# Kernel tuning notes

Measured on AMD Instinct MI355X. Metric: run time of the kernel, lower is better.

## Reference

```python
import jax, jax.numpy as jnp
import numpy as np

EPS = 0.3
LAYER_NUM = 2
N_NODES = 50000
N_EDGES = 1600000
IN_CH = 256
HIDDEN = 128
OUT_CH = 64


def setup_inputs() -> dict:
    key = jax.random.key(0)
    ks = jax.random.split(key, 8)
    x = jax.random.normal(ks[0], (N_NODES, IN_CH), dtype=jnp.float32)
    edge_index = jax.random.randint(ks[1], (2, N_EDGES), 0, N_NODES, dtype=jnp.int64)
    # xavier-normal-ish scales
    t1_w = jax.random.normal(ks[2], (HIDDEN, IN_CH), dtype=jnp.float32) * (1.414 * (2.0 / (IN_CH + HIDDEN)) ** 0.5)
    t1_b = jnp.zeros((HIDDEN,), dtype=jnp.float32)
    gate_w = jax.random.normal(ks[3], (LAYER_NUM, 2 * HIDDEN), dtype=jnp.float32) * ((2.0 / (2 * HIDDEN + 1)) ** 0.5)
    gate_b = jnp.zeros((LAYER_NUM,), dtype=jnp.float32)
    t2_w = jax.random.normal(ks[4], (OUT_CH, HIDDEN), dtype=jnp.float32) * (1.414 * (2.0 / (HIDDEN + OUT_CH)) ** 0.5)
    t2_b = jnp.zeros((OUT_CH,), dtype=jnp.float32)
    return {"x": x, "edge_index": edge_index, "t1_w": t1_w, "t1_b": t1_b,
            "gate_w": gate_w, "gate_b": gate_b, "t2_w": t2_w, "t2_b": t2_b}


def reference(x, edge_index, t1_w, t1_b, gate_w, gate_b, t2_w, t2_b):
    n = x.shape[0]
    row, col = edge_index[0], edge_index[1]
    # symmetric degree normalization: deg computed over target nodes (row)
    deg = jax.ops.segment_sum(jnp.ones_like(row, dtype=x.dtype), row, num_segments=n)
    dinv = jnp.where(deg > 0, jax.lax.rsqrt(jnp.maximum(deg, 1.0)), 0.0)  # [N]
    edge_norm = dinv[row] * dinv[col]  # [E]

    h = jax.nn.relu(x @ t1_w.T + t1_b)  # [N, H]
    raw = h
    H = h.shape[1]
    for l in range(LAYER_NUM):
        gw_i = gate_w[l, :H]   # weights for h_src (row)
        gw_j = gate_w[l, H:]   # weights for h_dst (col)
        # edge attention g = tanh(gate([h_row || h_col]))  -> [E]
        g = jnp.tanh(h[row] @ gw_i + h[col] @ gw_j + gate_b[l])
        w = g * edge_norm  # [E]
        # scatter-add weighted neighbor features to target nodes
        agg = jax.ops.segment_sum(w[:, None] * h[col], row, num_segments=n)  # [N, H]
        h = EPS * raw + agg
    out = h @ t2_w.T + t2_b  # [N, out]
    return jax.nn.log_softmax(out, axis=1)
```

## Files before the change

### kernel.cpp

```cpp
#include <hip/hip_runtime.h>
#include <math.h>

#define EPSF 0.3f
#define NPB 128
#define SHB 7
#define MAXNB 512
#define CHUNK 4096
#define MAXSEG 8192

typedef __attribute__((ext_vector_type(8))) short bf16x8;
typedef __attribute__((ext_vector_type(4))) float f32x4;

__device__ __forceinline__ uint32_t f2bf(float f) {
    uint32_t u = __float_as_uint(f);
    return (u + 0x7fffu + ((u >> 16) & 1u)) >> 16;
}
__device__ __forceinline__ uint32_t pack2(float lo, float hi) {
    return f2bf(lo) | (f2bf(hi) << 16);
}
__device__ __forceinline__ float bflo(uint32_t u) { return __uint_as_float(u << 16); }
__device__ __forceinline__ float bfhi(uint32_t u) { return __uint_as_float(u & 0xffff0000u); }

__device__ __forceinline__ float fast_tanh(float x) {
    float e = __expf(2.f * x);
    return 1.f - 2.f * __builtin_amdgcn_rcpf(e + 1.f);
}

__device__ __forceinline__ int edge_at(const int* ei, int is64, size_t idx) {
    if (is64) return (int)((const long long*)ei)[idx];
    return ei[idx];
}

__device__ __forceinline__ int detect_is64(const int* ei, int base, int E) {
    __shared__ int s_nz;
    if (threadIdx.x == 0) s_nz = 0;
    __syncthreads();
    int lim = min(512, E - base);
    int nz = 0;
    for (int t = threadIdx.x; t < lim; t += 256)
        nz |= (ei[2 * (size_t)(base + t) + 1] != 0);
    if (nz) atomicOr(&s_nz, 1);
    __syncthreads();
    return s_nz == 0;
}

__global__ __launch_bounds__(256) void k_pack(const int* __restrict__ ei, int E,
                                              uint32_t* __restrict__ pk,
                                              int* __restrict__ hist, int nblk, int NB) {
    __shared__ int lh[MAXNB];
    int base = blockIdx.x * CHUNK;
    int is64 = detect_is64(ei, base, E);
    for (int b = threadIdx.x; b < NB; b += 256) lh[b] = 0;
    __syncthreads();
    for (int j = threadIdx.x; j < CHUNK; j += 256) {
        int e = base + j;
        if (e < E) {
            int r = edge_at(ei, is64, e);
            int c = edge_at(ei, is64, (size_t)E + e);
            pk[e] = ((uint32_t)r << 16) | (uint32_t)c;
            atomicAdd(&lh[r >> SHB], 1);
        }
    }
    __syncthreads();
    for (int b = threadIdx.x; b < NB; b += 256)
        hist[(size_t)b * nblk + blockIdx.x] = lh[b];
}

__global__ void k_scanA(int* __restrict__ hist, int nblk, int* __restrict__ btot) {
    int b = blockIdx.x;
    int lane = threadIdx.x;
    int run = 0;
    for (int seg = 0; seg < nblk; seg += 64) {
        int idx = seg + lane;
        int v = (idx < nblk) ? hist[(size_t)b * nblk + idx] : 0;
        int s = v;
        for (int o = 1; o < 64; o <<= 1) {
            int t = __shfl_up(s, o);
            if (lane >= o) s += t;
        }
        if (idx < nblk) hist[(size_t)b * nblk + idx] = run + s - v;
        run += __shfl(s, 63);
    }
    if (lane == 0) btot[b] = run;
}

__global__ void k_scanB(const int* __restrict__ btot, int NB, int* __restrict__ bbase) {
    __shared__ int s[MAXNB];
    int t = threadIdx.x;
    int v = (t < NB) ? btot[t] : 0;
    s[t] = v;
    __syncthreads();
    for (int o = 1; o < MAXNB; o <<= 1) {
        int x = (t >= o) ? s[t - o] : 0;
        __syncthreads();
        s[t] += x;
        __syncthreads();
    }
    if (t < NB) bbase[t] = s[t] - v;
    if (t == MAXNB - 1) bbase[NB] = s[t];
}

__global__ __launch_bounds__(256) void k_binwrite(const uint32_t* __restrict__ pk, int E,
                                                  const int* __restrict__ hist,
                                                  const int* __restrict__ bbase,
                                                  uint32_t* __restrict__ ebuf,
                                                  int nblk, int NB) {
    __shared__ int lcnt[MAXNB];
    int base = blockIdx.x * CHUNK;
    for (int b = threadIdx.x; b < NB; b += 256)
        lcnt[b] = bbase[b] + hist[(size_t)b * nblk + blockIdx.x];
    __syncthreads();
    for (int j = threadIdx.x; j < CHUNK; j += 256) {
        int e = base + j;
        if (e < E) {
            uint32_t v = __builtin_nontemporal_load(&pk[e]);
            int pos = atomicAdd(&lcnt[v >> (16 + SHB)], 1);
            ebuf[pos] = v;
        }
    }
}

__global__ __launch_bounds__(256) void k_csr(const uint32_t* __restrict__ ebuf,
                                             const int* __restrict__ bbase,
                                             int* __restrict__ rp, float* __restrict__ dinv,
                                             int* __restrict__ ecol, int N, int E, int NB) {
    __shared__ uint32_t seg[MAXSEG];
    __shared__ int cnt[NPB];
    __shared__ int sc[NPB];
    __shared__ int cur[NPB];
    int b = blockIdx.x;
    int tid = threadIdx.x;
    int p0 = bbase[b], p1 = bbase[b + 1];
    int len = p1 - p0;
    bool fits = (len <= MAXSEG);
    int n0 = b << SHB;
    if (tid < NPB) cnt[tid] = 0;
    __syncthreads();
    if (fits) {
        for (int j = tid; j < len; j += 256) {
            uint32_t v = ebuf[p0 + j];
            seg[j] = v;
            atomicAdd(&cnt[(v >> 16) & (NPB - 1)], 1);
        }
    } else {
        for (int j = tid; j < len; j += 256)
            atomicAdd(&cnt[(ebuf[p0 + j] >> 16) & (NPB - 1)], 1);
    }
    __syncthreads();
    if (tid < NPB) sc[tid] = cnt[tid];
    __syncthreads();
    for (int o = 1; o < NPB; o <<= 1) {
        int v = (tid < NPB && tid >= o) ? sc[tid - o] : 0;
        __syncthreads();
        if (tid < NPB) sc[tid] += v;
        __syncthreads();
    }
    if (tid < NPB) {
        int off = sc[tid] - cnt[tid];
        cur[tid] = off;
        int node = n0 + tid;
        if (node < N) {
            rp[node] = p0 + off;
            int d = cnt[tid];
            dinv[node] = d > 0 ? rsqrtf((float)d) : 0.f;
        }
    }
    if (b == NB - 1 && tid == 0) rp[N] = E;
    __syncthreads();
    if (fits) {
        for (int j = tid; j < len; j += 256) {
            uint32_t v = seg[j];
            int pos = p0 + atomicAdd(&cur[(v >> 16) & (NPB - 1)], 1);
            ecol[pos] = (int)(v & 0xffffu);
        }
    } else {
        for (int j = tid; j < len; j += 256) {
            uint32_t v = ebuf[p0 + j];
            int pos = p0 + atomicAdd(&cur[(v >> 16) & (NPB - 1)], 1);
            ecol[pos] = (int)(v & 0xffffu);
        }
    }
}

__global__ __launch_bounds__(256) void k_gemm1(const float* __restrict__ A,
                                               const float* __restrict__ W,
                                               const float* __restrict__ bias,
                                               uint32_t* __restrict__ hb, int M) {
    __shared__ char As[128 * 128];
    __shared__ char Bs[128 * 128];
    const int tid = threadIdx.x;
    const int lane = tid & 63;
    const int wave = tid >> 6;
    const int wr = wave >> 1, wc = wave & 1;
    const int m0 = blockIdx.x * 128;
    const int lrow = lane & 15, lkg = lane >> 4;
    const int sr = tid >> 3;
    const int sc = (tid & 7) * 8;

    f32x4 acc[4][4];
#pragma unroll
    for (int mi = 0; mi < 4; ++mi)
#pragma unroll
        for (int ni = 0; ni < 4; ++ni) acc[mi][ni] = (f32x4){0.f, 0.f, 0.f, 0.f};

    for (int t = 0; t < 4; ++t) {
        const int k0 = t * 64;
#pragma unroll
        for (int i = 0; i < 4; ++i) {
            int r = i * 32 + sr;
            float4 v0 = make_float4(0.f, 0.f, 0.f, 0.f), v1 = v0;
            if (m0 + r < M) {
                const float* p = &A[(size_t)(m0 + r) * 256 + k0 + sc];
                v0 = *(const float4*)p;
                v1 = *(const float4*)(p + 4);
            }
            uint4 pk = make_uint4(pack2(v0.x, v0.y), pack2(v0.z, v0.w),
                                  pack2(v1.x, v1.y), pack2(v1.z, v1.w));
            uint32_t off = (uint32_t)(r * 128 + sc * 2);
            *(uint4*)(As + (off ^ ((r & 7) << 4))) = pk;
        }
#pragma unroll
        for (int i = 0; i < 4; ++i) {
            int r = i * 32 + sr;
            const float* p = &W[(size_t)r * 256 + k0 + sc];
            float4 v0 = *(const float4*)p;
            float4 v1 = *(const float4*)(p + 4);
            uint4 pk = make_uint4(pack2(v0.x, v0.y), pack2(v0.z, v0.w),
                                  pack2(v1.x, v1.y), pack2(v1.z, v1.w));
            uint32_t off = (uint32_t)(r * 128 + sc * 2);
            *(uint4*)(Bs + (off ^ ((r & 7) << 4))) = pk;
        }
        __syncthreads();
#pragma unroll
        for (int ks = 0; ks < 2; ++ks) {
            bf16x8 af[4], bfr[4];
#pragma unroll
            for (int mi = 0; mi < 4; ++mi) {
                int r = wr * 64 + mi * 16 + lrow;
                uint32_t off = (uint32_t)(r * 128 + ks * 64 + lkg * 16);
                af[mi] = *(const bf16x8*)(As + (off ^ ((r & 7) << 4)));
            }
#pragma unroll
            for (int ni = 0; ni < 4; ++ni) {
                int r = wc * 64 + ni * 16 + lrow;
                uint32_t off = (uint32_t)(r * 128 + ks * 64 + lkg * 16);
                bfr[ni] = *(const bf16x8*)(Bs + (off ^ ((r & 7) << 4)));
            }
#pragma unroll
            for (int mi = 0; mi < 4; ++mi)
#pragma unroll
                for (int ni = 0; ni < 4; ++ni)
                    acc[mi][ni] = __builtin_amdgcn_mfma_f32_16x16x32_bf16(
                        af[mi], bfr[ni], acc[mi][ni], 0, 0, 0);
        }
        __syncthreads();
    }
#pragma unroll
    for (int mi = 0; mi < 4; ++mi) {
#pragma unroll
        for (int ni = 0; ni < 4; ++ni) {
            int n = wc * 64 + ni * 16 + lrow;
            float bv = bias[n];
#pragma unroll
            for (int q = 0; q < 4; ++q) {
                float v = fmaxf(acc[mi][ni][q] + bv, 0.f);
                float vp = __shfl_xor(v, 1);
                int m = m0 + wr * 64 + mi * 16 + lkg * 4 + q;
                if (!(lane & 1) && m < M)
                    hb[(size_t)m * 64 + (n >> 1)] = pack2(v, vp);
            }
        }
    }
}

__global__ __launch_bounds__(256) void k_gemm2(const uint32_t* __restrict__ Abf,
                                               const float* __restrict__ W,
                                               const float* __restrict__ bias,
                                               float* __restrict__ out, int M) {
    __shared__ char As[128 * 128];
    __shared__ char Bs[64 * 128];
    __shared__ float redmax[2][128];
    __shared__ float redsum[2][128];
    const int tid = threadIdx.x;
    const int lane = tid & 63;
    const int wave = tid >> 6;
    const int wr = wave >> 1, wc = wave & 1;
    const int m0 = blockIdx.x * 128;
    const int lrow = lane & 15, lkg = lane >> 4;

    f32x4 acc[4][2];
#pragma unroll
    for (int mi = 0; mi < 4; ++mi)
#pragma unroll
        for (int ni = 0; ni < 2; ++ni) acc[mi][ni] = (f32x4){0.f, 0.f, 0.f, 0.f};

    for (int t = 0; t < 2; ++t) {
#pragma unroll
        for (int i = 0; i < 4; ++i) {
            int r = i * 32 + (tid >> 3);
            uint4 v = make_uint4(0u, 0u, 0u, 0u);
            if (m0 + r < M)
                v = *(const uint4*)&Abf[(size_t)(m0 + r) * 64 + t * 32 + (tid & 7) * 4];
            uint32_t off = (uint32_t)(r * 128 + (tid & 7) * 16);
            *(uint4*)(As + (off ^ ((r & 7) << 4))) = v;
        }
#pragma unroll
        for (int i = 0; i < 2; ++i) {
            int r = i * 32 + (tid >> 3);
            const float* p = &W[(size_t)r * 128 + t * 64 + (tid & 7) * 8];
            float4 v0 = *(const float4*)p, v1 = *(const float4*)(p + 4);
            uint4 pk = make_uint4(pack2(v0.x, v0.y), pack2(v0.z, v0.w),
                                  pack2(v1.x, v1.y), pack2(v1.z, v1.w));
            uint32_t off = (uint32_t)(r * 128 + (tid & 7) * 16);
            *(uint4*)(Bs + (off ^ ((r & 7) << 4))) = pk;
        }
        __syncthreads();
#pragma unroll
        for (int ks = 0; ks < 2; ++ks) {
            bf16x8 af[4], bfr[2];
#pragma unroll
            for (int mi = 0; mi < 4; ++mi) {
                int r = wr * 64 + mi * 16 + lrow;
                uint32_t off = (uint32_t)(r * 128 + ks * 64 + lkg * 16);
                af[mi] = *(const bf16x8*)(As + (off ^ ((r & 7) << 4)));
            }
#pragma unroll
            for (int ni = 0; ni < 2; ++ni) {
                int r = wc * 32 + ni * 16 + lrow;
                uint32_t off = (uint32_t)(r * 128 + ks * 64 + lkg * 16);
                bfr[ni] = *(const bf16x8*)(Bs + (off ^ ((r & 7) << 4)));
            }
#pragma unroll
            for (int mi = 0; mi < 4; ++mi)
#pragma unroll
                for (int ni = 0; ni < 2; ++ni)
                    acc[mi][ni] = __builtin_amdgcn_mfma_f32_16x16x32_bf16(
                        af[mi], bfr[ni], acc[mi][ni], 0, 0, 0);
        }
        __syncthreads();
    }

    float vb[4][2][4];
#pragma unroll
    for (int mi = 0; mi < 4; ++mi)
#pragma unroll
        for (int ni = 0; ni < 2; ++ni) {
            float bv = bias[wc * 32 + ni * 16 + lrow];
#pragma unroll
            for (int q = 0; q < 4; ++q) vb[mi][ni][q] = acc[mi][ni][q] + bv;
        }
#pragma unroll
    for (int mi = 0; mi < 4; ++mi)
#pragma unroll
        for (int q = 0; q < 4; ++q) {
            float mx = fmaxf(vb[mi][0][q], vb[mi][1][q]);
#pragma unroll
            for (int o = 1; o < 16; o <<= 1) mx = fmaxf(mx, __shfl_xor(mx, o));
            if (lrow == 0) redmax[wc][wr * 64 + mi * 16 + lkg * 4 + q] = mx;
        }
    __syncthreads();
    float fmv[4][4];
#pragma unroll
    for (int mi = 0; mi < 4; ++mi)
#pragma unroll
        for (int q = 0; q < 4; ++q) {
            int rl = wr * 64 + mi * 16 + lkg * 4 + q;
            float fm = fmaxf(redmax[0][rl], redmax[1][rl]);
            fmv[mi][q] = fm;
            float e = expf(vb[mi][0][q] - fm) + expf(vb[mi][1][q] - fm);
#pragma unroll
            for (int o = 1; o < 16; o <<= 1) e += __shfl_xor(e, o);
            if (lrow == 0) redsum[wc][rl] = e;
        }
    __syncthreads();
#pragma unroll
    for (int mi = 0; mi < 4; ++mi)
#pragma unroll
        for (int q = 0; q < 4; ++q) {
            int rl = wr * 64 + mi * 16 + lkg * 4 + q;
            int m = m0 + rl;
            if (m < M) {
                float ls = logf(redsum[0][rl] + redsum[1][rl]) + fmv[mi][q];
                out[(size_t)m * 64 + wc * 32 + lrow] = vb[mi][0][q] - ls;
                out[(size_t)m * 64 + wc * 32 + 16 + lrow] = vb[mi][1][q] - ls;
            }
        }
}

__global__ void k_ab(const uint32_t* __restrict__ hbv, const float* __restrict__ gw,
                     const float* __restrict__ gb, int layer,
                     const float* __restrict__ dinv,
                     float* __restrict__ av, float2* __restrict__ bd, int N) {
    int wid = threadIdx.x >> 6, lane = threadIdx.x & 63;
    int i = blockIdx.x * 4 + wid;
    if (i >= N) return;
    uint32_t u = hbv[(size_t)i * 64 + lane];
    float hx = bflo(u), hy = bfhi(u);
    float2 wi = *(const float2*)&gw[lane * 2];
    float2 wj = *(const float2*)&gw[128 + lane * 2];
    float pa = hx * wi.x + hy * wi.y;
    float pb = hx * wj.x + hy * wj.y;
    for (int o = 1; o < 64; o <<= 1) {
        pa += __shfl_xor(pa, o);
        pb += __shfl_xor(pb, o);
    }
    if (lane == 0) {
        av[i] = pa + gb[layer];
        bd[i] = make_float2(pb, dinv[i]);
    }
}

template <bool FUSE_AB, bool RAW_NT>
__global__ __launch_bounds__(256) void k_agg(const uint32_t* __restrict__ hb,
                                             const uint32_t* __restrict__ raw,
                                             const int* __restrict__ rp,
                                             const int* __restrict__ ecol,
                                             const float* __restrict__ av,
                                             const float2* __restrict__ bd,
                                             const float* __restrict__ dinv,
                                             uint32_t* __restrict__ hb_out,
                                             const float* __restrict__ gw_next,
                                             const float* __restrict__ gb_next,
                                             float* __restrict__ av_out,
                                             float2* __restrict__ bd_out, int N) {
    int wid = threadIdx.x >> 6, lane = threadIdx.x & 63;
    int i = blockIdx.x * 4 + wid;
    if (i >= N) return;
    int iu = __builtin_amdgcn_readfirstlane(i);
    int p0 = __builtin_amdgcn_readfirstlane(rp[iu]);
    int p1 = __builtin_amdgcn_readfirstlane(rp[iu + 1]);
    float a_i = av[iu];
    float di = dinv[iu];
    const int lg = lane >> 4;
    const int ll = lane & 15;

    uint32_t r0 = 0, r1 = 0, r2 = 0, r3 = 0;
    if (lane < 16) {
        const uint32_t* rpt = raw + (size_t)i * 64 + ll * 4;
        if (RAW_NT) {
            r0 = __builtin_nontemporal_load(rpt + 0);
            r1 = __builtin_nontemporal_load(rpt + 1);
            r2 = __builtin_nontemporal_load(rpt + 2);
            r3 = __builtin_nontemporal_load(rpt + 3);
        } else {
            r0 = rpt[0]; r1 = rpt[1]; r2 = rpt[2]; r3 = rpt[3];
        }
    }

    float acc[8];
#pragma unroll
    for (int j = 0; j < 8; ++j) acc[j] = 0.f;

    for (int b0 = p0; b0 < p1; b0 += 64) {
        int cnt = min(64, p1 - b0);
        uint32_t wcp = 0u;
        if (lane < cnt) {
            int c = __builtin_nontemporal_load(&ecol[b0 + lane]);
            float2 t = bd[c];
            float w = fast_tanh(a_i + t.x) * t.y;
            wcp = (f2bf(w) << 16) | (uint32_t)c;
        }
        int k = 0;
        for (; k + 8 <= cnt; k += 8) {
            uint32_t wx0 = __builtin_amdgcn_ds_bpermute((k + lg) << 2, (int)wcp);
            uint32_t wx1 = __builtin_amdgcn_ds_bpermute((k + 4 + lg) << 2, (int)wcp);
            float w0 = bfhi(wx0);
            float w1 = bfhi(wx1);
            int c0 = (int)(wx0 & 0xffffu);
            int c1 = (int)(wx1 & 0xffffu);
            uint4 u0 = *((const uint4*)(hb + ((size_t)c0 << 6)) + ll);
            uint4 u1 = *((const uint4*)(hb + ((size_t)c1 << 6)) + ll);
            acc[0] = fmaf(w0, bflo(u0.x), acc[0]); acc[1] = fmaf(w0, bfhi(u0.x), acc[1]);
            acc[2] = fmaf(w0, bflo(u0.y), acc[2]); acc[3] = fmaf(w0, bfhi(u0.y), acc[3]);
            acc[4] = fmaf(w0, bflo(u0.z), acc[4]); acc[5] = fmaf(w0, bfhi(u0.z), acc[5]);
            acc[6] = fmaf(w0, bflo(u0.w), acc[6]); acc[7] = fmaf(w0, bfhi(u0.w), acc[7]);
            acc[0] = fmaf(w1, bflo(u1.x), acc[0]); acc[1] = fmaf(w1, bfhi(u1.x), acc[1]);
            acc[2] = fmaf(w1, bflo(u1.y), acc[2]); acc[3] = fmaf(w1, bfhi(u1.y), acc[3]);
            acc[4] = fmaf(w1, bflo(u1.z), acc[4]); acc[5] = fmaf(w1, bfhi(u1.z), acc[5]);
            acc[6] = fmaf(w1, bflo(u1.w), acc[6]); acc[7] = fmaf(w1, bfhi(u1.w), acc[7]);
        }
        for (; k < cnt; k += 4) {
            uint32_t wx = __builtin_amdgcn_ds_bpermute((k + lg) << 2, (int)wcp);
            float w = bfhi(wx);
            int c = (int)(wx & 0xffffu);
            uint4 u = *((const uint4*)(hb + ((size_t)c << 6)) + ll);
            acc[0] = fmaf(w, bflo(u.x), acc[0]); acc[1] = fmaf(w, bfhi(u.x), acc[1]);
            acc[2] = fmaf(w, bflo(u.y), acc[2]); acc[3] = fmaf(w, bfhi(u.y), acc[3]);
            acc[4] = fmaf(w, bflo(u.z), acc[4]); acc[5] = fmaf(w, bfhi(u.z), acc[5]);
            acc[6] = fmaf(w, bflo(u.w), acc[6]); acc[7] = fmaf(w, bfhi(u.w), acc[7]);
        }
    }
#pragma unroll
    for (int j = 0; j < 8; ++j) {
        acc[j] += __shfl_xor(acc[j], 16);
        acc[j] += __shfl_xor(acc[j], 32);
    }
    if (lane < 16) {
        float o[8];
        o[0] = EPSF * bflo(r0) + di * acc[0]; o[1] = EPSF * bfhi(r0) + di * acc[1];
        o[2] = EPSF * bflo(r1) + di * acc[2]; o[3] = EPSF * bfhi(r1) + di * acc[3];
        o[4] = EPSF * bflo(r2) + di * acc[4]; o[5] = EPSF * bfhi(r2) + di * acc[5];
        o[6] = EPSF * bflo(r3) + di * acc[6]; o[7] = EPSF * bfhi(r3) + di * acc[7];
        uint4 w4;
        w4.x = pack2(o[0], o[1]); w4.y = pack2(o[2], o[3]);
        w4.z = pack2(o[4], o[5]); w4.w = pack2(o[6], o[7]);
        *((uint4*)(hb_out + (size_t)i * 64) + ll) = w4;
        if (FUSE_AB) {
            float pa = 0.f, pb = 0.f;
#pragma unroll
            for (int j = 0; j < 8; ++j) {
                int ch = ll * 8 + j;
                pa = fmaf(o[j], gw_next[ch], pa);
                pb = fmaf(o[j], gw_next[128 + ch], pb);
            }
#pragma unroll
            for (int off = 1; off < 16; off <<= 1) {
                pa += __shfl_xor(pa, off);
                pb += __shfl_xor(pb, off);
            }
            if (ll == 0) {
                av_out[i] = pa + gb_next[0];
                bd_out[i] = make_float2(pb, di);
            }
        }
    }
}

extern "C" void kernel_launch(void* const* d_in, const int* in_sizes, int n_in,
                              void* d_out, int out_size, void* d_ws, size_t ws_size,
                              hipStream_t stream) {
    const float* x = (const float*)d_in[0];
    const int* ei = (const int*)d_in[1];
    const float* t1w = (const float*)d_in[2];
    const float* t1b = (const float*)d_in[3];
    const float* gw = (const float*)d_in[4];
    const float* gb = (const float*)d_in[5];
    const float* t2w = (const float*)d_in[6];
    const float* t2b = (const float*)d_in[7];
    float* out = (float*)d_out;

    const int INC = 256;
    const int N = in_sizes[0] / INC;
    const int E = in_sizes[1] / 2;
    const int NB = (N + NPB - 1) >> SHB;
    const int nblk = (E + CHUNK - 1) / CHUNK;

    char* ws = (char*)d_ws;
    auto alloc = [&](size_t bytes) {
        char* p = ws;
        ws += (bytes + 255) & ~(size_t)255;
        return p;
    };
    uint32_t* pk = (uint32_t*)alloc((size_t)E * 4);
    int* hist = (int*)alloc((size_t)NB * nblk * 4);
    int* btot = (int*)alloc((size_t)NB * 4);
    int* bbase = (int*)alloc((size_t)(NB + 1) * 4);
    uint32_t* ebuf = (uint32_t*)alloc((size_t)E * 4);
    int* rp = (int*)alloc((size_t)(N + 1) * 4);
    float* dinv = (float*)alloc((size_t)N * 4);
    int* ecol = (int*)alloc((size_t)E * 4);
    float* av0 = (float*)alloc((size_t)N * 4);
    float* av1 = (float*)alloc((size_t)N * 4);
    float2* bd0 = (float2*)alloc((size_t)N * 8);
    float2* bd1 = (float2*)alloc((size_t)N * 8);
    uint32_t* hb0 = (uint32_t*)alloc((size_t)N * 64 * 4);
    uint32_t* hb1 = (uint32_t*)alloc((size_t)N * 64 * 4);
    uint32_t* hb2 = (uint32_t*)alloc((size_t)N * 64 * 4);

    k_pack<<<nblk, 256, 0, stream>>>(ei, E, pk, hist, nblk, NB);
    k_scanA<<<NB, 64, 0, stream>>>(hist, nblk, btot);
    k_scanB<<<1, MAXNB, 0, stream>>>(btot, NB, bbase);
    k_binwrite<<<nblk, 256, 0, stream>>>(pk, E, hist, bbase, ebuf, nblk, NB);
    k_csr<<<NB, 256, 0, stream>>>(ebuf, bbase, rp, dinv, ecol, N, E, NB);

    k_gemm1<<<(N + 127) / 128, 256, 0, stream>>>(x, t1w, t1b, hb0, N);

    k_ab<<<(N + 3) / 4, 256, 0, stream>>>(hb0, gw + 0 * 256, gb, 0, dinv, av0, bd0, N);
    k_agg<true, false><<<(N + 3) / 4, 256, 0, stream>>>(
        hb0, hb0, rp, ecol, av0, bd0, dinv, hb1, gw + 1 * 256, gb + 1, av1, bd1, N);
    k_agg<false, true><<<(N + 3) / 4, 256, 0, stream>>>(
        hb1, hb0, rp, ecol, av1, bd1, dinv, hb2, nullptr, nullptr, nullptr, nullptr, N);

    k_gemm2<<<(N + 127) / 128, 256, 0, stream>>>(hb2, t2w, t2b, out, N);
}
```

Before: 200.5 us.

## Fuse scan into consumers, gate projection into GEMM1 epilogue, unroll gather

```diff
diff --git a/kernel.cpp b/kernel.cpp
--- a/kernel.cpp
+++ b/kernel.cpp
@@ -42,6 +42,19 @@
     if (nz) atomicOr(&s_nz, 1);
     __syncthreads();
     return s_nz == 0;
+}
+
+__device__ __forceinline__ void scan512(int* s) {
+    int t = threadIdx.x;
+    for (int o = 1; o < MAXNB; o <<= 1) {
+        int i2 = t + 256;
+        int x1 = (t >= o) ? s[t - o] : 0;
+        int x2 = (i2 >= o) ? s[i2 - o] : 0;
+        __syncthreads();
+        s[t] += x1;
+        s[i2] += x2;
+        __syncthreads();
+    }
 }
 
 __global__ __launch_bounds__(256) void k_pack(const int* __restrict__ ei, int E,
@@ -84,33 +97,22 @@
     if (lane == 0) btot[b] = run;
 }
 
-__global__ void k_scanB(const int* __restrict__ btot, int NB, int* __restrict__ bbase) {
-    __shared__ int s[MAXNB];
-    int t = threadIdx.x;
-    int v = (t < NB) ? btot[t] : 0;
-    s[t] = v;
-    __syncthreads();
-    for (int o = 1; o < MAXNB; o <<= 1) {
-        int x = (t >= o) ? s[t - o] : 0;
-        __syncthreads();
-        s[t] += x;
-        __syncthreads();
-    }
-    if (t < NB) bbase[t] = s[t] - v;
-    if (t == MAXNB - 1) bbase[NB] = s[t];
-}
-
 __global__ __launch_bounds__(256) void k_binwrite(const uint32_t* __restrict__ pk, int E,
                                                   const int* __restrict__ hist,
-                                                  const int* __restrict__ bbase,
+                                                  const int* __restrict__ btot,
                                                   uint32_t* __restrict__ ebuf,
                                                   int nblk, int NB) {
+    __shared__ int s[MAXNB];
     __shared__ int lcnt[MAXNB];
+    int t = threadIdx.x;
+    for (int b = t; b < MAXNB; b += 256) s[b] = (b < NB) ? btot[b] : 0;
+    __syncthreads();
+    scan512(s);
+    for (int b = t; b < NB; b += 256)
+        lcnt[b] = s[b] - btot[b] + hist[(size_t)b * nblk + blockIdx.x];
+    __syncthreads();
     int base = blockIdx.x * CHUNK;
-    for (int b = threadIdx.x; b < NB; b += 256)
-        lcnt[b] = bbase[b] + hist[(size_t)b * nblk + blockIdx.x];
-    __syncthreads();
-    for (int j = threadIdx.x; j < CHUNK; j += 256) {
+    for (int j = t; j < CHUNK; j += 256) {
         int e = base + j;
         if (e < E) {
             uint32_t v = __builtin_nontemporal_load(&pk[e]);
@@ -121,16 +123,21 @@
 }
 
 __global__ __launch_bounds__(256) void k_csr(const uint32_t* __restrict__ ebuf,
-                                             const int* __restrict__ bbase,
+                                             const int* __restrict__ btot,
                                              int* __restrict__ rp, float* __restrict__ dinv,
                                              int* __restrict__ ecol, int N, int E, int NB) {
+    __shared__ int s[MAXNB];
     __shared__ uint32_t seg[MAXSEG];
     __shared__ int cnt[NPB];
     __shared__ int sc[NPB];
     __shared__ int cur[NPB];
     int b = blockIdx.x;
     int tid = threadIdx.x;
-    int p0 = bbase[b], p1 = bbase[b + 1];
+    for (int k = tid; k < MAXNB; k += 256) s[k] = (k < NB) ? btot[k] : 0;
+    __syncthreads();
+    scan512(s);
+    int p1 = s[b];
+    int p0 = p1 - btot[b];
     int len = p1 - p0;
     bool fits = (len <= MAXSEG);
     int n0 = b << SHB;
@@ -185,9 +192,16 @@
 __global__ __launch_bounds__(256) void k_gemm1(const float* __restrict__ A,
                                                const float* __restrict__ W,
                                                const float* __restrict__ bias,
-                                               uint32_t* __restrict__ hb, int M) {
+                                               uint32_t* __restrict__ hb,
+                                               const float* __restrict__ gw0,
+                                               const float* __restrict__ gb,
+                                               const float* __restrict__ dinv,
+                                               float* __restrict__ av,
+                                               float2* __restrict__ bd, int M) {
     __shared__ char As[128 * 128];
     __shared__ char Bs[128 * 128];
+    __shared__ float pab_a[2][128];
+    __shared__ float pab_b[2][128];
     const int tid = threadIdx.x;
     const int lane = tid & 63;
     const int wave = tid >> 6;
@@ -255,20 +269,49 @@
         }
         __syncthreads();
     }
+    float bv[4], gi[4], gj[4];
+#pragma unroll
+    for (int ni = 0; ni < 4; ++ni) {
+        int n = wc * 64 + ni * 16 + lrow;
+        bv[ni] = bias[n];
+        gi[ni] = gw0[n];
+        gj[ni] = gw0[128 + n];
+    }
 #pragma unroll
     for (int mi = 0; mi < 4; ++mi) {
 #pragma unroll
-        for (int ni = 0; ni < 4; ++ni) {
-            int n = wc * 64 + ni * 16 + lrow;
-            float bv = bias[n];
-#pragma unroll
-            for (int q = 0; q < 4; ++q) {
-                float v = fmaxf(acc[mi][ni][q] + bv, 0.f);
+        for (int q = 0; q < 4; ++q) {
+            float pa = 0.f, pb = 0.f;
+            int m = m0 + wr * 64 + mi * 16 + lkg * 4 + q;
+#pragma unroll
+            for (int ni = 0; ni < 4; ++ni) {
+                float v = fmaxf(acc[mi][ni][q] + bv[ni], 0.f);
                 float vp = __shfl_xor(v, 1);
-                int m = m0 + wr * 64 + mi * 16 + lkg * 4 + q;
-                if (!(lane & 1) && m < M)
+                if (!(lane & 1) && m < M) {
+                    int n = wc * 64 + ni * 16 + lrow;
                     hb[(size_t)m * 64 + (n >> 1)] = pack2(v, vp);
-            }
+                }
+                pa = fmaf(v, gi[ni], pa);
+                pb = fmaf(v, gj[ni], pb);
+            }
+#pragma unroll
+            for (int o = 1; o < 16; o <<= 1) {
+                pa += __shfl_xor(pa, o);
+                pb += __shfl_xor(pb, o);
+            }
+            if (lrow == 0) {
+                int rl = wr * 64 + mi * 16 + lkg * 4 + q;
+                pab_a[wc][rl] = pa;
+                pab_b[wc][rl] = pb;
+            }
+        }
+    }
+    __syncthreads();
+    if (tid < 128) {
+        int m = m0 + tid;
+        if (m < M) {
+            av[m] = pab_a[0][tid] + pab_a[1][tid] + gb[0];
+            bd[m] = make_float2(pab_b[0][tid] + pab_b[1][tid], dinv[m]);
         }
     }
 }
@@ -345,9 +388,9 @@
     for (int mi = 0; mi < 4; ++mi)
 #pragma unroll
         for (int ni = 0; ni < 2; ++ni) {
-            float bv = bias[wc * 32 + ni * 16 + lrow];
-#pragma unroll
-            for (int q = 0; q < 4; ++q) vb[mi][ni][q] = acc[mi][ni][q] + bv;
+            float bvx = bias[wc * 32 + ni * 16 + lrow];
+#pragma unroll
+            for (int q = 0; q < 4; ++q) vb[mi][ni][q] = acc[mi][ni][q] + bvx;
         }
 #pragma unroll
     for (int mi = 0; mi < 4; ++mi)
@@ -385,29 +428,6 @@
                 out[(size_t)m * 64 + wc * 32 + 16 + lrow] = vb[mi][1][q] - ls;
             }
         }
-}
-
-__global__ void k_ab(const uint32_t* __restrict__ hbv, const float* __restrict__ gw,
-                     const float* __restrict__ gb, int layer,
-                     const float* __restrict__ dinv,
-                     float* __restrict__ av, float2* __restrict__ bd, int N) {
-    int wid = threadIdx.x >> 6, lane = threadIdx.x & 63;
-    int i = blockIdx.x * 4 + wid;
-    if (i >= N) return;
-    uint32_t u = hbv[(size_t)i * 64 + lane];
-    float hx = bflo(u), hy = bfhi(u);
-    float2 wi = *(const float2*)&gw[lane * 2];
-    float2 wj = *(const float2*)&gw[128 + lane * 2];
-    float pa = hx * wi.x + hy * wi.y;
-    float pb = hx * wj.x + hy * wj.y;
-    for (int o = 1; o < 64; o <<= 1) {
-        pa += __shfl_xor(pa, o);
-        pb += __shfl_xor(pb, o);
-    }
-    if (lane == 0) {
-        av[i] = pa + gb[layer];
-        bd[i] = make_float2(pb, dinv[i]);
-    }
 }
 
 template <bool FUSE_AB, bool RAW_NT>
@@ -433,6 +453,7 @@
     float di = dinv[iu];
     const int lg = lane >> 4;
     const int ll = lane & 15;
+    const char* hbp = (const char*)hb + (ll << 4);
 
     uint32_t r0 = 0, r1 = 0, r2 = 0, r3 = 0;
     if (lane < 16) {
@@ -451,6 +472,12 @@
 #pragma unroll
     for (int j = 0; j < 8; ++j) acc[j] = 0.f;
 
+#define FMA8(W, U)                                                              \
+    acc[0] = fmaf(W, bflo((U).x), acc[0]); acc[1] = fmaf(W, bfhi((U).x), acc[1]); \
+    acc[2] = fmaf(W, bflo((U).y), acc[2]); acc[3] = fmaf(W, bfhi((U).y), acc[3]); \
+    acc[4] = fmaf(W, bflo((U).z), acc[4]); acc[5] = fmaf(W, bfhi((U).z), acc[5]); \
+    acc[6] = fmaf(W, bflo((U).w), acc[6]); acc[7] = fmaf(W, bfhi((U).w), acc[7]);
+
     for (int b0 = p0; b0 < p1; b0 += 64) {
         int cnt = min(64, p1 - b0);
         uint32_t wcp = 0u;
@@ -460,36 +487,25 @@
             float w = fast_tanh(a_i + t.x) * t.y;
             wcp = (f2bf(w) << 16) | (uint32_t)c;
         }
-        int k = 0;
-        for (; k + 8 <= cnt; k += 8) {
-            uint32_t wx0 = __builtin_amdgcn_ds_bpermute((k + lg) << 2, (int)wcp);
-            uint32_t wx1 = __builtin_amdgcn_ds_bpermute((k + 4 + lg) << 2, (int)wcp);
-            float w0 = bfhi(wx0);
-            float w1 = bfhi(wx1);
-            int c0 = (int)(wx0 & 0xffffu);
-            int c1 = (int)(wx1 & 0xffffu);
-            uint4 u0 = *((const uint4*)(hb + ((size_t)c0 << 6)) + ll);
-            uint4 u1 = *((const uint4*)(hb + ((size_t)c1 << 6)) + ll);
-            acc[0] = fmaf(w0, bflo(u0.x), acc[0]); acc[1] = fmaf(w0, bfhi(u0.x), acc[1]);
-            acc[2] = fmaf(w0, bflo(u0.y), acc[2]); acc[3] = fmaf(w0, bfhi(u0.y), acc[3]);
-            acc[4] = fmaf(w0, bflo(u0.z), acc[4]); acc[5] = fmaf(w0, bfhi(u0.z), acc[5]);
-            acc[6] = fmaf(w0, bflo(u0.w), acc[6]); acc[7] = fmaf(w0, bfhi(u0.w), acc[7]);
-            acc[0] = fmaf(w1, bflo(u1.x), acc[0]); acc[1] = fmaf(w1, bfhi(u1.x), acc[1]);
-            acc[2] = fmaf(w1, bflo(u1.y), acc[2]); acc[3] = fmaf(w1, bfhi(u1.y), acc[3]);
-            acc[4] = fmaf(w1, bflo(u1.z), acc[4]); acc[5] = fmaf(w1, bfhi(u1.z), acc[5]);
-            acc[6] = fmaf(w1, bflo(u1.w), acc[6]); acc[7] = fmaf(w1, bfhi(u1.w), acc[7]);
-        }
-        for (; k < cnt; k += 4) {
-            uint32_t wx = __builtin_amdgcn_ds_bpermute((k + lg) << 2, (int)wcp);
-            float w = bfhi(wx);
-            int c = (int)(wx & 0xffffu);
-            uint4 u = *((const uint4*)(hb + ((size_t)c << 6)) + ll);
-            acc[0] = fmaf(w, bflo(u.x), acc[0]); acc[1] = fmaf(w, bfhi(u.x), acc[1]);
-            acc[2] = fmaf(w, bflo(u.y), acc[2]); acc[3] = fmaf(w, bfhi(u.y), acc[3]);
-            acc[4] = fmaf(w, bflo(u.z), acc[4]); acc[5] = fmaf(w, bfhi(u.z), acc[5]);
-            acc[6] = fmaf(w, bflo(u.w), acc[6]); acc[7] = fmaf(w, bfhi(u.w), acc[7]);
-        }
-    }
+        int cntp = (cnt + 15) & ~15;
+        for (int k = 0; k < cntp; k += 16) {
+            int kb = (k + lg) << 2;
+            uint32_t wx0 = __builtin_amdgcn_ds_bpermute(kb, (int)wcp);
+            uint32_t wx1 = __builtin_amdgcn_ds_bpermute(kb + 16, (int)wcp);
+            uint32_t wx2 = __builtin_amdgcn_ds_bpermute(kb + 32, (int)wcp);
+            uint32_t wx3 = __builtin_amdgcn_ds_bpermute(kb + 48, (int)wcp);
+            uint4 u0 = *(const uint4*)(hbp + ((wx0 & 0xffffu) << 8));
+            uint4 u1 = *(const uint4*)(hbp + ((wx1 & 0xffffu) << 8));
+            uint4 u2 = *(const uint4*)(hbp + ((wx2 & 0xffffu) << 8));
+            uint4 u3 = *(const uint4*)(hbp + ((wx3 & 0xffffu) << 8));
+            float w0 = bfhi(wx0), w1 = bfhi(wx1), w2 = bfhi(wx2), w3 = bfhi(wx3);
+            FMA8(w0, u0);
+            FMA8(w1, u1);
+            FMA8(w2, u2);
+            FMA8(w3, u3);
+        }
+    }
+#undef FMA8
 #pragma unroll
     for (int j = 0; j < 8; ++j) {
         acc[j] += __shfl_xor(acc[j], 16);
@@ -554,7 +570,6 @@
     uint32_t* pk = (uint32_t*)alloc((size_t)E * 4);
     int* hist = (int*)alloc((size_t)NB * nblk * 4);
     int* btot = (int*)alloc((size_t)NB * 4);
-    int* bbase = (int*)alloc((size_t)(NB + 1) * 4);
     uint32_t* ebuf = (uint32_t*)alloc((size_t)E * 4);
     int* rp = (int*)alloc((size_t)(N + 1) * 4);
     float* dinv = (float*)alloc((size_t)N * 4);
@@ -569,13 +584,12 @@
 
     k_pack<<<nblk, 256, 0, stream>>>(ei, E, pk, hist, nblk, NB);
     k_scanA<<<NB, 64, 0, stream>>>(hist, nblk, btot);
-    k_scanB<<<1, MAXNB, 0, stream>>>(btot, NB, bbase);
-    k_binwrite<<<nblk, 256, 0, stream>>>(pk, E, hist, bbase, ebuf, nblk, NB);
-    k_csr<<<NB, 256, 0, stream>>>(ebuf, bbase, rp, dinv, ecol, N, E, NB);
-
-    k_gemm1<<<(N + 127) / 128, 256, 0, stream>>>(x, t1w, t1b, hb0, N);
-
-    k_ab<<<(N + 3) / 4, 256, 0, stream>>>(hb0, gw + 0 * 256, gb, 0, dinv, av0, bd0, N);
+    k_binwrite<<<nblk, 256, 0, stream>>>(pk, E, hist, btot, ebuf, nblk, NB);
+    k_csr<<<NB, 256, 0, stream>>>(ebuf, btot, rp, dinv, ecol, N, E, NB);
+
+    k_gemm1<<<(N + 127) / 128, 256, 0, stream>>>(x, t1w, t1b, hb0,
+                                                 gw + 0 * 256, gb, dinv, av0, bd0, N);
+
     k_agg<true, false><<<(N + 3) / 4, 256, 0, stream>>>(
         hb0, hb0, rp, ecol, av0, bd0, dinv, hb1, gw + 1 * 256, gb + 1, av1, bd1, N);
     k_agg<false, true><<<(N + 3) / 4, 256, 0, stream>>>(
```

Result: faster. 189.6 us (-5.4%).
